# Kernel optimization log

Hardware: AMD Instinct MI355X
Metric: run time of the kernel (lower is better)

The kernel has to match this reference:

```python
import jax, jax.numpy as jnp
import numpy as np

N = 200000      # query points
D_IN = 3        # coordinate dims
H = 256         # hidden features
L = 4           # hidden layers (between first and last Perceptron)
S = 8           # n_series == out_features


def setup_inputs() -> dict:
    key = jax.random.key(0)
    ks = jax.random.split(key, 7)
    coords = jax.random.normal(ks[0], (N, D_IN), dtype=jnp.float32)
    # Stacked per-series weights (all series share shapes; original loads the
    # same checkpoint into each, but we use independent random params).
    scale0 = 1.0 / np.sqrt(D_IN)
    scaleh = 1.0 / np.sqrt(H)
    W0 = jax.random.uniform(ks[1], (S, D_IN, H), jnp.float32, -scale0, scale0)
    b0 = jax.random.uniform(ks[2], (S, H), jnp.float32, -scale0, scale0)
    Wh = jax.random.uniform(ks[3], (S, L, H, H), jnp.float32, -scaleh, scaleh)
    bh = jax.random.uniform(ks[4], (S, L, H), jnp.float32, -scaleh, scaleh)
    Wout = jax.random.uniform(ks[5], (S, H, 1), jnp.float32, -scaleh, scaleh)
    bout = jax.random.uniform(ks[6], (S, 1), jnp.float32, -scaleh, scaleh)
    return {"coords": coords, "W0": W0, "b0": b0, "Wh": Wh, "bh": bh,
            "Wout": Wout, "bout": bout}


def reference(coords, W0, b0, Wh, bh, Wout, bout):
    # All S series' MLPs batched into grouped GEMMs (einsum over series axis s).
    # Perceptron = Linear + softplus; last layer is plain Linear.
    h = jax.nn.softplus(jnp.einsum('nd,sdh->snh', coords, W0) + b0[:, None, :])
    for i in range(L):  # small fixed layer count
        h = jax.nn.softplus(
            jnp.einsum('snh,shk->snk', h, Wh[:, i]) + bh[:, i][:, None, :])
    out = jnp.einsum('snh,sho->sno', h, Wout) + bout[:, None, :]  # [S,N,1]
    output = jnp.transpose(out[..., 0], (1, 0))  # concat along dim=1 -> [N,S]
    return (output, coords)
```

## Files before the change

kernel.cpp:

```cpp
#include <hip/hip_runtime.h>
#include <hip/hip_bf16.h>
#include <cstdint>

typedef __attribute__((ext_vector_type(8))) short short8;
typedef __attribute__((ext_vector_type(4))) float float4v;

#define LOG2E 1.44269504088896340736f
#define LN2   0.69314718055994530942f

#if __has_builtin(__builtin_amdgcn_exp2f)
__device__ __forceinline__ float fexp2(float x){ return __builtin_amdgcn_exp2f(x); }
#else
__device__ __forceinline__ float fexp2(float x){ return exp2f(x); }
#endif
#if __has_builtin(__builtin_amdgcn_logf)
__device__ __forceinline__ float flog2(float x){ return __builtin_amdgcn_logf(x); }
#else
__device__ __forceinline__ float flog2(float x){ return log2f(x); }
#endif

__device__ __forceinline__ float softplus_hat(float zh){
  return flog2(1.0f + fexp2(zh));
}

__device__ __forceinline__ unsigned short bf16_trunc(float f){
  return (unsigned short)(__builtin_bit_cast(unsigned int, f) >> 16);
}

#define HSTRIDE 264

__global__ void convert_wh(const float* __restrict__ Wh,
                           unsigned short* __restrict__ Wt){
  int e = blockIdx.x * 256 + threadIdx.x;
  int n  = e & 255;
  int k  = (e >> 8) & 255;
  int sl = e >> 16;
  float v = Wh[e];
  __hip_bfloat16 h = __float2bfloat16(v);
  Wt[(sl << 16) + ((k >> 5) << 13) + (n << 5) + (k & 31)] =
      __builtin_bit_cast(unsigned short, h);
}

__device__ __forceinline__ float4v bf16_mfma(short8 a, short8 b, float4v c){
  return __builtin_amdgcn_mfma_f32_16x16x32_bf16(a, b, c, 0, 0, 0);
}

template<int L>
__device__ __forceinline__ void hidden_mfma(
    const unsigned short* __restrict__ bbase0,
    const unsigned short* __restrict__ aptr,
    short8 (&bq)[3][4], float4v (&acc)[4][4])
{
  const unsigned short* bb = bbase0 + L * 65536;
  const unsigned short* bn = bbase0 + (L + 1) * 65536;

  short8 a0[4], a1[4];
  #pragma unroll
  for (int mi = 0; mi < 4; ++mi)
    a0[mi] = *(const short8*)(aptr + mi * 4224);

  #pragma unroll
  for (int kb = 0; kb < 8; ++kb) {
    short8* cur = (kb & 1) ? a1 : a0;
    short8* nxt = (kb & 1) ? a0 : a1;
    if (kb < 7) {
      #pragma unroll
      for (int mi = 0; mi < 4; ++mi)
        nxt[mi] = *(const short8*)(aptr + mi * 4224 + (kb + 1) * 32);
    }
    const int slot = (8 * L + kb) % 3;
    #pragma unroll
    for (int mi = 0; mi < 4; ++mi)
      #pragma unroll
      for (int ni = 0; ni < 4; ++ni)
        acc[mi][ni] = bf16_mfma(cur[mi], bq[slot][ni], acc[mi][ni]);
    if (kb < 5) {
      #pragma unroll
      for (int ni = 0; ni < 4; ++ni)
        bq[slot][ni] = *(const short8*)(bb + (kb + 3) * 8192 + ni * 512);
    } else if (L < 3) {
      #pragma unroll
      for (int ni = 0; ni < 4; ++ni)
        bq[slot][ni] = *(const short8*)(bn + (kb - 5) * 8192 + ni * 512);
    }
  }
}

__global__ __launch_bounds__(256, 2) void series_mlp(
    const float* __restrict__ coords,
    const float* __restrict__ W0, const float* __restrict__ b0,
    const float* __restrict__ bh,
    const float* __restrict__ Wout, const float* __restrict__ bout,
    const unsigned short* __restrict__ Wt,
    float* __restrict__ out)
{
  __shared__ __align__(16) unsigned short h_lds[64 * HSTRIDE];
  __shared__ float cbuf[192];

  const int tid  = threadIdx.x;
  const int lane = tid & 63;
  const int wave = tid >> 6;
  const int s    = blockIdx.x & 7;
  const int m0   = (blockIdx.x >> 3) * 64;

  if (tid < 192) cbuf[tid] = coords[m0 * 3 + tid];
  __syncthreads();

  {
    const int c  = tid;
    const float w0 = W0[(s * 3 + 0) * 256 + c] * LOG2E;
    const float w1 = W0[(s * 3 + 1) * 256 + c] * LOG2E;
    const float w2 = W0[(s * 3 + 2) * 256 + c] * LOG2E;
    const float bb = b0[s * 256 + c] * LOG2E;
    const float4v* c4 = (const float4v*)cbuf;
    #pragma unroll
    for (int j = 0; j < 16; ++j) {
      float4v x0 = c4[j * 3 + 0];
      float4v x1 = c4[j * 3 + 1];
      float4v x2 = c4[j * 3 + 2];
      float z0 = fmaf(x0.z, w2, fmaf(x0.y, w1, fmaf(x0.x, w0, bb)));
      float z1 = fmaf(x1.y, w2, fmaf(x1.x, w1, fmaf(x0.w, w0, bb)));
      float z2 = fmaf(x2.x, w2, fmaf(x1.w, w1, fmaf(x1.z, w0, bb)));
      float z3 = fmaf(x2.w, w2, fmaf(x2.z, w1, fmaf(x2.y, w0, bb)));
      h_lds[(4 * j + 0) * HSTRIDE + c] = bf16_trunc(softplus_hat(z0));
      h_lds[(4 * j + 1) * HSTRIDE + c] = bf16_trunc(softplus_hat(z1));
      h_lds[(4 * j + 2) * HSTRIDE + c] = bf16_trunc(softplus_hat(z2));
      h_lds[(4 * j + 3) * HSTRIDE + c] = bf16_trunc(softplus_hat(z3));
    }
  }
  __syncthreads();

  const int colb = (wave << 6) + (lane & 15);
  const int q    = lane >> 4;
  const unsigned short* aptr = h_lds + (lane & 15) * HSTRIDE + q * 8;
  unsigned short* cptr = h_lds + (q * 4) * HSTRIDE + colb;

  const unsigned short* bbase0 = Wt + ((s << 2) << 16) + (colb << 5) + (q << 3);

  short8 bq[3][4];
  #pragma unroll
  for (int i = 0; i < 3; ++i)
    #pragma unroll
    for (int ni = 0; ni < 4; ++ni)
      bq[i][ni] = *(const short8*)(bbase0 + i * 8192 + ni * 512);

  float4v acc[4][4];

  #define HIDDEN_LAYER(L)                                                     \
  {                                                                           \
    float bias[4];                                                            \
    _Pragma("unroll")                                                         \
    for (int ni = 0; ni < 4; ++ni)                                            \
      bias[ni] = bh[((s << 2) + L) * 256 + colb + ni * 16] * LOG2E;           \
    _Pragma("unroll")                                                         \
    for (int mi = 0; mi < 4; ++mi)                                            \
      _Pragma("unroll")                                                       \
      for (int ni = 0; ni < 4; ++ni)                                          \
        acc[mi][ni] = (float4v){bias[ni], bias[ni], bias[ni], bias[ni]};      \
    hidden_mfma<L>(bbase0, aptr, bq, acc);                                    \
    _Pragma("unroll")                                                         \
    for (int mi = 0; mi < 4; ++mi)                                            \
      _Pragma("unroll")                                                       \
      for (int ni = 0; ni < 4; ++ni) {                                        \
        float4v v = acc[mi][ni];                                              \
        _Pragma("unroll")                                                     \
        for (int r = 0; r < 4; ++r) v[r] = softplus_hat(v[r]);                \
        acc[mi][ni] = v;                                                      \
      }                                                                       \
    __syncthreads();                                                          \
    _Pragma("unroll")                                                         \
    for (int mi = 0; mi < 4; ++mi)                                            \
      _Pragma("unroll")                                                       \
      for (int ni = 0; ni < 4; ++ni) {                                        \
        float4v v = acc[mi][ni];                                              \
        _Pragma("unroll")                                                     \
        for (int r = 0; r < 4; ++r)                                           \
          cptr[mi * 4224 + r * HSTRIDE + ni * 16] = bf16_trunc(v[r]);         \
      }                                                                       \
    __syncthreads();                                                          \
  }

  HIDDEN_LAYER(0)
  HIDDEN_LAYER(1)
  HIDDEN_LAYER(2)
  #undef HIDDEN_LAYER

  {
    float bias[4];
    #pragma unroll
    for (int ni = 0; ni < 4; ++ni)
      bias[ni] = bh[((s << 2) + 3) * 256 + colb + ni * 16] * LOG2E;
    #pragma unroll
    for (int mi = 0; mi < 4; ++mi)
      #pragma unroll
      for (int ni = 0; ni < 4; ++ni)
        acc[mi][ni] = (float4v){bias[ni], bias[ni], bias[ni], bias[ni]};

    hidden_mfma<3>(bbase0, aptr, bq, acc);

    float wv[4];
    #pragma unroll
    for (int ni = 0; ni < 4; ++ni)
      wv[ni] = Wout[(s << 8) + colb + ni * 16];
    float p[16];
    #pragma unroll
    for (int i = 0; i < 16; ++i) p[i] = 0.f;
    #pragma unroll
    for (int mi = 0; mi < 4; ++mi)
      #pragma unroll
      for (int ni = 0; ni < 4; ++ni) {
        float4v v = acc[mi][ni];
        #pragma unroll
        for (int r = 0; r < 4; ++r)
          p[mi * 4 + r] = fmaf(softplus_hat(v[r]), wv[ni], p[mi * 4 + r]);
      }

    __syncthreads();
    float* red = (float*)h_lds;
    #pragma unroll
    for (int mi = 0; mi < 4; ++mi)
      #pragma unroll
      for (int r = 0; r < 4; ++r) {
        int row = mi * 16 + (q << 2) + r;
        red[row * 68 + (wave << 4) + (lane & 15)] = p[mi * 4 + r];
      }
    __syncthreads();

    if (tid < 64) {
      const float4v* rr = (const float4v*)&red[tid * 68];
      float4v a = rr[0];
      #pragma unroll
      for (int i = 1; i < 16; ++i) {
        float4v b = rr[i];
        a.x += b.x; a.y += b.y; a.z += b.z; a.w += b.w;
      }
      float tot = (a.x + a.y) + (a.z + a.w);
      out[(m0 + tid) * 8 + s] = fmaf(LN2, tot, bout[s]);
    }
  }
}

__global__ __launch_bounds__(256) void series_mlp_slow(
    const float* __restrict__ coords,
    const float* __restrict__ W0, const float* __restrict__ b0,
    const float* __restrict__ Wh, const float* __restrict__ bh,
    const float* __restrict__ Wout, const float* __restrict__ bout,
    float* __restrict__ out)
{
  __shared__ float h[64 * 256];
  __shared__ float cbuf[192];
  __shared__ float red[256];
  const int tid = threadIdx.x;
  const int s   = blockIdx.y;
  const int m0  = blockIdx.x * 64;

  if (tid < 192) cbuf[tid] = coords[m0 * 3 + tid];
  __syncthreads();
  {
    const float w0 = W0[(s * 3 + 0) * 256 + tid];
    const float w1 = W0[(s * 3 + 1) * 256 + tid];
    const float w2 = W0[(s * 3 + 2) * 256 + tid];
    const float bb = b0[s * 256 + tid];
    for (int m = 0; m < 64; ++m) {
      float z = fmaf(cbuf[m * 3 + 2], w2,
                fmaf(cbuf[m * 3 + 1], w1,
                fmaf(cbuf[m * 3 + 0], w0, bb)));
      h[m * 256 + tid] = LN2 * softplus_hat(z * LOG2E);
    }
  }
  __syncthreads();

  for (int l = 0; l < 4; ++l) {
    const float* W = Wh + (((s << 2) + l) << 16);
    const float bb = bh[((s << 2) + l) * 256 + tid];
    float acc[64];
    #pragma unroll
    for (int m = 0; m < 64; ++m) acc[m] = bb;
    for (int kc = 0; kc < 64; ++kc) {
      float w0 = W[(kc * 4 + 0) * 256 + tid];
      float w1 = W[(kc * 4 + 1) * 256 + tid];
      float w2 = W[(kc * 4 + 2) * 256 + tid];
      float w3 = W[(kc * 4 + 3) * 256 + tid];
      #pragma unroll
      for (int m = 0; m < 64; ++m) {
        float4v hv = *(const float4v*)&h[m * 256 + kc * 4];
        acc[m] = fmaf(hv.w, w3, fmaf(hv.z, w2,
                 fmaf(hv.y, w1, fmaf(hv.x, w0, acc[m]))));
      }
    }
    __syncthreads();
    #pragma unroll
    for (int m = 0; m < 64; ++m)
      h[m * 256 + tid] = LN2 * softplus_hat(acc[m] * LOG2E);
    __syncthreads();
  }
  {
    const int m = tid >> 2, qq = tid & 3;
    const float* wv = Wout + (s << 8);
    float sum = 0.f;
    for (int i = 0; i < 16; ++i) {
      int kk = (qq << 6) + ((((tid & 15) + i) << 2) & 63);
      float4v hv = *(const float4v*)&h[m * 256 + kk];
      sum += hv.x * wv[kk] + hv.y * wv[kk + 1] + hv.z * wv[kk + 2] + hv.w * wv[kk + 3];
    }
    red[tid] = sum;
    __syncthreads();
    if (tid < 64)
      out[(m0 + tid) * 8 + s] =
          red[tid * 4] + red[tid * 4 + 1] + red[tid * 4 + 2] + red[tid * 4 + 3] + bout[s];
  }
}

extern "C" void kernel_launch(void* const* d_in, const int* in_sizes, int n_in,
                              void* d_out, int out_size, void* d_ws, size_t ws_size,
                              hipStream_t stream) {
  const float* coords = (const float*)d_in[0];
  const float* W0     = (const float*)d_in[1];
  const float* b0     = (const float*)d_in[2];
  const float* Wh     = (const float*)d_in[3];
  const float* bh     = (const float*)d_in[4];
  const float* Wout   = (const float*)d_in[5];
  const float* bout   = (const float*)d_in[6];
  float* out = (float*)d_out;

  const size_t WT_BYTES = (size_t)8 * 4 * 256 * 256 * 2;
  if (ws_size >= WT_BYTES) {
    unsigned short* Wt = (unsigned short*)d_ws;
    convert_wh<<<8192, 256, 0, stream>>>(Wh, Wt);
    series_mlp<<<dim3(25000), dim3(256), 0, stream>>>(
        coords, W0, b0, bh, Wout, bout, Wt, out);
  } else {
    series_mlp_slow<<<dim3(3125, 8), dim3(256), 0, stream>>>(
        coords, W0, b0, Wh, bh, Wout, bout, out);
  }
  hipMemcpyAsync(out + (size_t)200000 * 8, coords,
                 (size_t)200000 * 3 * sizeof(float),
                 hipMemcpyDeviceToDevice, stream);
}
```

Before: 916.0 us.

## Swap MFMA operands to transpose accumulator layout for packed LDS stores and shuffle reduction

Swaps the A/B operands of the bf16 MFMA so each lane's accumulator holds four consecutive hidden features of one row instead of four rows of one feature. This lets the activations be packed into 64-bit bf16 stores to LDS, and lets the bias and output weights be loaded as float4 vectors. The final dot-product reduction now uses cross-lane shuffles plus a small shared buffer instead of a 64x68 LDS scratch pass. The LDS row stride changes to 260, which changes the bank-conflict pattern of the A-operand reads.

```diff
diff --git a/kernel.cpp b/kernel.cpp
--- a/kernel.cpp
+++ b/kernel.cpp
@@ -4,6 +4,7 @@
 
 typedef __attribute__((ext_vector_type(8))) short short8;
 typedef __attribute__((ext_vector_type(4))) float float4v;
+typedef __attribute__((ext_vector_type(2))) unsigned int uint2v;
 
 #define LOG2E 1.44269504088896340736f
 #define LN2   0.69314718055994530942f
@@ -23,11 +24,15 @@
   return flog2(1.0f + fexp2(zh));
 }
 
+__device__ __forceinline__ unsigned int pack_bf16(float lo, float hi){
+  return (__builtin_bit_cast(unsigned int, hi) & 0xFFFF0000u) |
+         (__builtin_bit_cast(unsigned int, lo) >> 16);
+}
 __device__ __forceinline__ unsigned short bf16_trunc(float f){
   return (unsigned short)(__builtin_bit_cast(unsigned int, f) >> 16);
 }
 
-#define HSTRIDE 264
+#define HSTRIDE 260
 
 __global__ void convert_wh(const float* __restrict__ Wh,
                            unsigned short* __restrict__ Wt){
@@ -57,7 +62,7 @@
   short8 a0[4], a1[4];
   #pragma unroll
   for (int mi = 0; mi < 4; ++mi)
-    a0[mi] = *(const short8*)(aptr + mi * 4224);
+    a0[mi] = *(const short8*)(aptr + mi * 4160);
 
   #pragma unroll
   for (int kb = 0; kb < 8; ++kb) {
@@ -66,14 +71,14 @@
     if (kb < 7) {
       #pragma unroll
       for (int mi = 0; mi < 4; ++mi)
-        nxt[mi] = *(const short8*)(aptr + mi * 4224 + (kb + 1) * 32);
+        nxt[mi] = *(const short8*)(aptr + (kb + 1) * 32 + mi * 4160);
     }
     const int slot = (8 * L + kb) % 3;
     #pragma unroll
     for (int mi = 0; mi < 4; ++mi)
       #pragma unroll
       for (int ni = 0; ni < 4; ++ni)
-        acc[mi][ni] = bf16_mfma(cur[mi], bq[slot][ni], acc[mi][ni]);
+        acc[mi][ni] = bf16_mfma(bq[slot][ni], cur[mi], acc[mi][ni]);
     if (kb < 5) {
       #pragma unroll
       for (int ni = 0; ni < 4; ++ni)
@@ -96,10 +101,11 @@
 {
   __shared__ __align__(16) unsigned short h_lds[64 * HSTRIDE];
   __shared__ float cbuf[192];
+  __shared__ float red2[256];
 
   const int tid  = threadIdx.x;
   const int lane = tid & 63;
-  const int wave = tid >> 6;
+  const int wn   = tid >> 6;
   const int s    = blockIdx.x & 7;
   const int m0   = (blockIdx.x >> 3) * 64;
 
@@ -130,10 +136,10 @@
   }
   __syncthreads();
 
-  const int colb = (wave << 6) + (lane & 15);
+  const int colb = (wn << 6) + (lane & 15);
   const int q    = lane >> 4;
   const unsigned short* aptr = h_lds + (lane & 15) * HSTRIDE + q * 8;
-  unsigned short* cptr = h_lds + (q * 4) * HSTRIDE + colb;
+  unsigned short* cptr = h_lds + (lane & 15) * HSTRIDE + (wn << 6) + (q << 2);
 
   const unsigned short* bbase0 = Wt + ((s << 2) << 16) + (colb << 5) + (q << 3);
 
@@ -145,38 +151,40 @@
       bq[i][ni] = *(const short8*)(bbase0 + i * 8192 + ni * 512);
 
   float4v acc[4][4];
+  const float* bh_s = bh + (s << 10);
+  const int nb = (wn << 6) + (q << 2);
 
   #define HIDDEN_LAYER(L)                                                     \
   {                                                                           \
-    float bias[4];                                                            \
+    float4v bias4[4];                                                         \
     _Pragma("unroll")                                                         \
-    for (int ni = 0; ni < 4; ++ni)                                            \
-      bias[ni] = bh[((s << 2) + L) * 256 + colb + ni * 16] * LOG2E;           \
+    for (int ni = 0; ni < 4; ++ni) {                                          \
+      float4v b = *(const float4v*)&bh_s[L * 256 + nb + ni * 16];             \
+      b.x *= LOG2E; b.y *= LOG2E; b.z *= LOG2E; b.w *= LOG2E;                 \
+      bias4[ni] = b;                                                          \
+    }                                                                         \
     _Pragma("unroll")                                                         \
     for (int mi = 0; mi < 4; ++mi)                                            \
       _Pragma("unroll")                                                       \
       for (int ni = 0; ni < 4; ++ni)                                          \
-        acc[mi][ni] = (float4v){bias[ni], bias[ni], bias[ni], bias[ni]};      \
+        acc[mi][ni] = bias4[ni];                                              \
     hidden_mfma<L>(bbase0, aptr, bq, acc);                                    \
+    uint2v pk[4][4];                                                          \
     _Pragma("unroll")                                                         \
     for (int mi = 0; mi < 4; ++mi)                                            \
       _Pragma("unroll")                                                       \
       for (int ni = 0; ni < 4; ++ni) {                                        \
         float4v v = acc[mi][ni];                                              \
-        _Pragma("unroll")                                                     \
-        for (int r = 0; r < 4; ++r) v[r] = softplus_hat(v[r]);                \
-        acc[mi][ni] = v;                                                      \
+        float s0 = softplus_hat(v.x), s1 = softplus_hat(v.y);                 \
+        float s2 = softplus_hat(v.z), s3 = softplus_hat(v.w);                 \
+        pk[mi][ni] = (uint2v){pack_bf16(s0, s1), pack_bf16(s2, s3)};          \
       }                                                                       \
     __syncthreads();                                                          \
     _Pragma("unroll")                                                         \
     for (int mi = 0; mi < 4; ++mi)                                            \
       _Pragma("unroll")                                                       \
-      for (int ni = 0; ni < 4; ++ni) {                                        \
-        float4v v = acc[mi][ni];                                              \
-        _Pragma("unroll")                                                     \
-        for (int r = 0; r < 4; ++r)                                           \
-          cptr[mi * 4224 + r * HSTRIDE + ni * 16] = bf16_trunc(v[r]);         \
-      }                                                                       \
+      for (int ni = 0; ni < 4; ++ni)                                          \
+        *(uint2v*)(cptr + mi * 4160 + ni * 16) = pk[mi][ni];                  \
     __syncthreads();                                                          \
   }
 
@@ -186,55 +194,52 @@
   #undef HIDDEN_LAYER
 
   {
-    float bias[4];
+    float4v bias4[4];
+    #pragma unroll
+    for (int ni = 0; ni < 4; ++ni) {
+      float4v b = *(const float4v*)&bh_s[3 * 256 + nb + ni * 16];
+      b.x *= LOG2E; b.y *= LOG2E; b.z *= LOG2E; b.w *= LOG2E;
+      bias4[ni] = b;
+    }
+    #pragma unroll
+    for (int mi = 0; mi < 4; ++mi)
+      #pragma unroll
+      for (int ni = 0; ni < 4; ++ni)
+        acc[mi][ni] = bias4[ni];
+
+    hidden_mfma<3>(bbase0, aptr, bq, acc);
+
+    float4v wv4[4];
     #pragma unroll
     for (int ni = 0; ni < 4; ++ni)
-      bias[ni] = bh[((s << 2) + 3) * 256 + colb + ni * 16] * LOG2E;
-    #pragma unroll
-    for (int mi = 0; mi < 4; ++mi)
-      #pragma unroll
-      for (int ni = 0; ni < 4; ++ni)
-        acc[mi][ni] = (float4v){bias[ni], bias[ni], bias[ni], bias[ni]};
-
-    hidden_mfma<3>(bbase0, aptr, bq, acc);
-
-    float wv[4];
-    #pragma unroll
-    for (int ni = 0; ni < 4; ++ni)
-      wv[ni] = Wout[(s << 8) + colb + ni * 16];
-    float p[16];
-    #pragma unroll
-    for (int i = 0; i < 16; ++i) p[i] = 0.f;
+      wv4[ni] = *(const float4v*)&Wout[(s << 8) + nb + ni * 16];
+
+    float pd[4] = {0.f, 0.f, 0.f, 0.f};
     #pragma unroll
     for (int mi = 0; mi < 4; ++mi)
       #pragma unroll
       for (int ni = 0; ni < 4; ++ni) {
         float4v v = acc[mi][ni];
-        #pragma unroll
-        for (int r = 0; r < 4; ++r)
-          p[mi * 4 + r] = fmaf(softplus_hat(v[r]), wv[ni], p[mi * 4 + r]);
+        pd[mi] = fmaf(softplus_hat(v.x), wv4[ni].x,
+                 fmaf(softplus_hat(v.y), wv4[ni].y,
+                 fmaf(softplus_hat(v.z), wv4[ni].z,
+                 fmaf(softplus_hat(v.w), wv4[ni].w, pd[mi]))));
       }
 
+    #pragma unroll
+    for (int mi = 0; mi < 4; ++mi) {
+      pd[mi] += __shfl_xor(pd[mi], 16, 64);
+      pd[mi] += __shfl_xor(pd[mi], 32, 64);
+    }
+    if (lane < 16) {
+      #pragma unroll
+      for (int mi = 0; mi < 4; ++mi)
+        red2[(wn << 6) + mi * 16 + lane] = pd[mi];
+    }
     __syncthreads();
-    float* red = (float*)h_lds;
-    #pragma unroll
-    for (int mi = 0; mi < 4; ++mi)
-      #pragma unroll
-      for (int r = 0; r < 4; ++r) {
-        int row = mi * 16 + (q << 2) + r;
-        red[row * 68 + (wave << 4) + (lane & 15)] = p[mi * 4 + r];
-      }
-    __syncthreads();
 
     if (tid < 64) {
-      const float4v* rr = (const float4v*)&red[tid * 68];
-      float4v a = rr[0];
-      #pragma unroll
-      for (int i = 1; i < 16; ++i) {
-        float4v b = rr[i];
-        a.x += b.x; a.y += b.y; a.z += b.z; a.w += b.w;
-      }
-      float tot = (a.x + a.y) + (a.z + a.w);
+      float tot = red2[tid] + red2[64 + tid] + red2[128 + tid] + red2[192 + tid];
       out[(m0 + tid) * 8 + s] = fmaf(LN2, tot, bout[s]);
     }
   }
@@ -247,7 +252,7 @@
     const float* __restrict__ Wout, const float* __restrict__ bout,
     float* __restrict__ out)
 {
-  __shared__ float h[64 * 256];
+  __shared__ float hh[64 * 256];
   __shared__ float cbuf[192];
   __shared__ float red[256];
   const int tid = threadIdx.x;
@@ -265,7 +270,7 @@
       float z = fmaf(cbuf[m * 3 + 2], w2,
                 fmaf(cbuf[m * 3 + 1], w1,
                 fmaf(cbuf[m * 3 + 0], w0, bb)));
-      h[m * 256 + tid] = LN2 * softplus_hat(z * LOG2E);
+      hh[m * 256 + tid] = LN2 * softplus_hat(z * LOG2E);
     }
   }
   __syncthreads();
@@ -283,7 +288,7 @@
       float w3 = W[(kc * 4 + 3) * 256 + tid];
       #pragma unroll
       for (int m = 0; m < 64; ++m) {
-        float4v hv = *(const float4v*)&h[m * 256 + kc * 4];
+        float4v hv = *(const float4v*)&hh[m * 256 + kc * 4];
         acc[m] = fmaf(hv.w, w3, fmaf(hv.z, w2,
                  fmaf(hv.y, w1, fmaf(hv.x, w0, acc[m]))));
       }
@@ -291,7 +296,7 @@
     __syncthreads();
     #pragma unroll
     for (int m = 0; m < 64; ++m)
-      h[m * 256 + tid] = LN2 * softplus_hat(acc[m] * LOG2E);
+      hh[m * 256 + tid] = LN2 * softplus_hat(acc[m] * LOG2E);
     __syncthreads();
   }
   {
@@ -300,7 +305,7 @@
     float sum = 0.f;
     for (int i = 0; i < 16; ++i) {
       int kk = (qq << 6) + ((((tid & 15) + i) << 2) & 63);
-      float4v hv = *(const float4v*)&h[m * 256 + kk];
+      float4v hv = *(const float4v*)&hh[m * 256 + kk];
       sum += hv.x * wv[kk] + hv.y * wv[kk + 1] + hv.z * wv[kk + 2] + hv.w * wv[kk + 3];
     }
     red[tid] = sum;
```

Result: slower. 1.700 ms (+85.6%).
